# Performance work log

Measured on AMD Instinct MI355X. Metric: run time of the kernel, lower is better.

The kernel has to match this reference:

```python
import jax, jax.numpy as jnp
import numpy as np

B, L, D, V1, V2, V3 = 512, 48, 256, 512, 512, 64


def setup_inputs() -> dict:
    key = jax.random.key(0)
    ks = jax.random.split(key, 20)
    def w(k, shape, fan_in):
        return jax.random.normal(k, shape, dtype=jnp.float32) / np.sqrt(fan_in)
    inp = {
        'x1': jax.random.normal(ks[0], (B, L, V1), dtype=jnp.float32),
        'x2': jax.random.normal(ks[1], (B, L, V2), dtype=jnp.float32),
        's': jax.random.normal(ks[2], (B, V3), dtype=jnp.float32),
        'w_e1': w(ks[3], (D, V1), V1), 'b_e1': jnp.zeros((D,), jnp.float32),
        'w_e2': w(ks[4], (D, V2), V2), 'b_e2': jnp.zeros((D,), jnp.float32),
        'w_s': w(ks[5], (D, V3), V3), 'b_s': jnp.zeros((D,), jnp.float32),
        'w_x': w(ks[6], (1, D), D),                      # mlp_for_x, no bias
        'w_h': w(ks[7], (L, D), D), 'b_h': w(ks[8], (L,), D),  # mlp_for_hidden
        'w_ih': w(ks[9], (3 * D, D), D), 'w_hh': w(ks[10], (3 * D, D), D),
        'b_ih': w(ks[11], (3 * D,), D), 'b_hh': w(ks[12], (3 * D,), D),
        'w_out': w(ks[13], (1, D), D), 'b_out': jnp.zeros((1,), jnp.float32),
    }
    return inp


def _gru_cell(x, h, w_ih, w_hh, b_ih, b_hh):
    # torch GRUCell: gates ordered r, z, n
    gi = x @ w_ih.T + b_ih
    gh = h @ w_hh.T + b_hh
    i_r, i_z, i_n = jnp.split(gi, 3, axis=-1)
    h_r, h_z, h_n = jnp.split(gh, 3, axis=-1)
    r = jax.nn.sigmoid(i_r + h_r)
    z = jax.nn.sigmoid(i_z + h_z)
    n = jnp.tanh(i_n + r * h_n)
    return (1.0 - z) * n + z * h


def reference(x1, x2, s, w_e1, b_e1, w_e2, b_e2, w_s, b_s, w_x, w_h, b_h,
              w_ih, w_hh, b_ih, b_hh, w_out, b_out):
    x1e = jax.nn.relu(jnp.einsum('blv,dv->bld', x1, w_e1) + b_e1)
    x2e = jax.nn.relu(jnp.einsum('blv,dv->bld', x2, w_e2) + b_e2)
    se = s @ w_s.T + b_s                      # [B, D]
    x = x1e + x2e                             # [B, L, D]
    # prefix[:, i] = sum_{j < i} x2e[:, j, 0]  (the torch.where zero test)
    cums = jnp.cumsum(x2e[:, :, 0], axis=1)
    prefix = jnp.concatenate([jnp.zeros((B, 1), x.dtype), cums[:, :-1]], axis=1)  # [B, L]
    idx = jnp.arange(L)

    def step(h, inputs):
        i, pref = inputs                       # i: scalar step, pref: [B]
        le = (idx <= i).astype(x.dtype)        # keep timesteps 0..i (pad rest with 0)
        ip = x * le[None, :, None]             # input_padded [B, L, D]
        lt = (idx < i)
        cond = (pref == 0.0)[:, None]          # batches with zero history in ch0
        guid = jnp.where(idx[None, :] == i, 1.0,
                         jnp.where(cond & lt[None, :], 1.0, 0.0)).astype(x.dtype)  # [B, L]
        gi = ip * guid[:, :, None]
        t1 = jnp.einsum('bld,d->bl', gi, w_x[0]) + (h @ w_h.T + b_h)  # [B, L]
        a = jax.nn.softmax(t1, axis=1)
        ctx = jnp.einsum('bld,bl->bd', ip, a)
        h2 = _gru_cell(ctx, h, w_ih, w_hh, b_ih, b_hh)
        return h2, None

    h0 = jnp.zeros((B, D), x.dtype)
    hF, _ = jax.lax.scan(step, h0, (idx, prefix.T))
    y = jax.nn.sigmoid((hF + se) @ w_out.T + b_out)  # [B, 1]
    return y
```

## Files before the change

### kernel.cpp

```cpp
#include <hip/hip_runtime.h>
#include <stdint.h>

#define B_ 512
#define L_ 48
#define D_ 256

typedef __attribute__((ext_vector_type(8))) short bf16x8;
typedef __attribute__((ext_vector_type(4))) short bf16x4;
typedef __attribute__((ext_vector_type(4))) float f32x4;
typedef __attribute__((ext_vector_type(4))) int i32x4;

__device__ __forceinline__ short f2bf(float f) {
    union { float f; unsigned u; } v; v.f = f;
    unsigned u = v.u;
    unsigned r = (u + 0x7FFFu + ((u >> 16) & 1u)) >> 16;
    return (short)r;
}
__device__ __forceinline__ float bf2f(short s) {
    union { unsigned u; float f; } v; v.u = ((unsigned)(unsigned short)s) << 16;
    return v.f;
}

__global__ __launch_bounds__(256) void k_prep(const float* __restrict__ w_hh,
                                              const float* __restrict__ w_h,
                                              const float* __restrict__ w_ih,
                                              signed char* __restrict__ W1q,
                                              signed char* __restrict__ W2q,
                                              float* __restrict__ qA,
                                              float* __restrict__ qC) {
    int w = threadIdx.x >> 6, lane = threadIdx.x & 63;
    int R = blockIdx.x * 4 + w;
    if (R >= 1584) return;
    const float* src;
    signed char* dst;
    bool isA = (R < 816);
    if (R < 768)      { src = w_hh + (size_t)R * 256;         dst = W1q + (size_t)R * 256; }
    else if (R < 816) { src = w_h + (size_t)(R - 768) * 256;  dst = W1q + (size_t)R * 256; }
    else              { src = w_ih + (size_t)(R - 816) * 256; dst = W2q + (size_t)(R - 816) * 256; }
    float4 v = *(const float4*)(src + lane * 4);
    float m = fmaxf(fmaxf(fabsf(v.x), fabsf(v.y)), fmaxf(fabsf(v.z), fabsf(v.w)));
    #pragma unroll
    for (int o = 32; o; o >>= 1) m = fmaxf(m, __shfl_xor(m, o));
    float sc = (m > 0.f) ? 127.f / m : 0.f;
    int b0 = __float2int_rn(v.x * sc), b1 = __float2int_rn(v.y * sc);
    int b2 = __float2int_rn(v.z * sc), b3 = __float2int_rn(v.w * sc);
    unsigned word = (unsigned)(b0 & 255) | ((unsigned)(b1 & 255) << 8) |
                    ((unsigned)(b2 & 255) << 16) | ((unsigned)(b3 & 255) << 24);
    ((unsigned*)dst)[lane] = word;
    if (lane == 0) {
        if (isA) qA[R] = m / (127.f * 127.f);
        else     qC[R - 816] = m * 8.f / (127.f * 127.f);
    }
}

__device__ __forceinline__ void gemm_pass(const float* __restrict__ X,
                                          const float* __restrict__ W,
                                          short (*sA)[40], short (*sB)[40],
                                          int m0, int n0, int srow, int sseg,
                                          int mf, int nf, int row16, int kg,
                                          f32x4 (&acc)[2][4]) {
    for (int k0 = 0; k0 < 512; k0 += 32) {
        __syncthreads();
        {
            const float* src = X + (size_t)(m0 + srow) * 512 + k0 + sseg * 8;
            float4 p0 = *(const float4*)(src);
            float4 p1 = *(const float4*)(src + 4);
            bf16x8 v;
            v[0] = f2bf(p0.x); v[1] = f2bf(p0.y); v[2] = f2bf(p0.z); v[3] = f2bf(p0.w);
            v[4] = f2bf(p1.x); v[5] = f2bf(p1.y); v[6] = f2bf(p1.z); v[7] = f2bf(p1.w);
            *(bf16x8*)&sA[srow][sseg * 8] = v;
        }
        {
            const float* src = W + (size_t)(n0 + srow) * 512 + k0 + sseg * 8;
            float4 p0 = *(const float4*)(src);
            float4 p1 = *(const float4*)(src + 4);
            bf16x8 v;
            v[0] = f2bf(p0.x); v[1] = f2bf(p0.y); v[2] = f2bf(p0.z); v[3] = f2bf(p0.w);
            v[4] = f2bf(p1.x); v[5] = f2bf(p1.y); v[6] = f2bf(p1.z); v[7] = f2bf(p1.w);
            *(bf16x8*)&sB[srow][sseg * 8] = v;
        }
        __syncthreads();
        bf16x8 a0 = *(bf16x8*)&sA[(mf + 0) * 16 + row16][kg * 8];
        bf16x8 a1 = *(bf16x8*)&sA[(mf + 1) * 16 + row16][kg * 8];
        #pragma unroll
        for (int j = 0; j < 4; ++j) {
            bf16x8 bv = *(bf16x8*)&sB[(nf + j) * 16 + row16][kg * 8];
            acc[0][j] = __builtin_amdgcn_mfma_f32_16x16x32_bf16(a0, bv, acc[0][j], 0, 0, 0);
            acc[1][j] = __builtin_amdgcn_mfma_f32_16x16x32_bf16(a1, bv, acc[1][j], 0, 0, 0);
        }
    }
}

__device__ __forceinline__ void gemm_pass_c0(const float* __restrict__ X,
                                             const float* __restrict__ W,
                                             const float* __restrict__ we2r0,
                                             bool doC0, float& c0acc,
                                             short (*sA)[40], short (*sB)[40],
                                             int m0, int n0, int srow, int sseg,
                                             int mf, int nf, int row16, int kg,
                                             f32x4 (&acc)[2][4]) {
    for (int k0 = 0; k0 < 512; k0 += 32) {
        __syncthreads();
        {
            const float* src = X + (size_t)(m0 + srow) * 512 + k0 + sseg * 8;
            float4 p0 = *(const float4*)(src);
            float4 p1 = *(const float4*)(src + 4);
            if (doC0) {
                const float* wr = we2r0 + k0 + sseg * 8;
                c0acc += p0.x * wr[0] + p0.y * wr[1] + p0.z * wr[2] + p0.w * wr[3]
                       + p1.x * wr[4] + p1.y * wr[5] + p1.z * wr[6] + p1.w * wr[7];
            }
            bf16x8 v;
            v[0] = f2bf(p0.x); v[1] = f2bf(p0.y); v[2] = f2bf(p0.z); v[3] = f2bf(p0.w);
            v[4] = f2bf(p1.x); v[5] = f2bf(p1.y); v[6] = f2bf(p1.z); v[7] = f2bf(p1.w);
            *(bf16x8*)&sA[srow][sseg * 8] = v;
        }
        {
            const float* src = W + (size_t)(n0 + srow) * 512 + k0 + sseg * 8;
            float4 p0 = *(const float4*)(src);
            float4 p1 = *(const float4*)(src + 4);
            bf16x8 v;
            v[0] = f2bf(p0.x); v[1] = f2bf(p0.y); v[2] = f2bf(p0.z); v[3] = f2bf(p0.w);
            v[4] = f2bf(p1.x); v[5] = f2bf(p1.y); v[6] = f2bf(p1.z); v[7] = f2bf(p1.w);
            *(bf16x8*)&sB[srow][sseg * 8] = v;
        }
        __syncthreads();
        bf16x8 a0 = *(bf16x8*)&sA[(mf + 0) * 16 + row16][kg * 8];
        bf16x8 a1 = *(bf16x8*)&sA[(mf + 1) * 16 + row16][kg * 8];
        #pragma unroll
        for (int j = 0; j < 4; ++j) {
            bf16x8 bv = *(bf16x8*)&sB[(nf + j) * 16 + row16][kg * 8];
            acc[0][j] = __builtin_amdgcn_mfma_f32_16x16x32_bf16(a0, bv, acc[0][j], 0, 0, 0);
            acc[1][j] = __builtin_amdgcn_mfma_f32_16x16x32_bf16(a1, bv, acc[1][j], 0, 0, 0);
        }
    }
}

__global__ __launch_bounds__(512) void k_embed(const float* __restrict__ x1,
                                               const float* __restrict__ x2,
                                               const float* __restrict__ w_e1,
                                               const float* __restrict__ b_e1,
                                               const float* __restrict__ w_e2,
                                               const float* __restrict__ b_e2,
                                               short* __restrict__ xb,
                                               float* __restrict__ c0) {
    __shared__ short sA[128][40];
    __shared__ short sB[128][40];
    int bid = blockIdx.x;
    int mt = bid >> 1, nt = bid & 1;
    int m0 = mt * 128, n0 = nt * 128;
    int tid = threadIdx.x;
    int lane = tid & 63, w = tid >> 6;
    int mf = (w & 3) * 2;
    int nf = (w >> 2) * 4;
    int row16 = lane & 15, kg = lane >> 4;
    int srow = tid >> 2, sseg = tid & 3;

    f32x4 acc[2][4], keep[2][4];
    #pragma unroll
    for (int a = 0; a < 2; ++a)
        #pragma unroll
        for (int j = 0; j < 4; ++j) { acc[a][j] = {0.f, 0.f, 0.f, 0.f}; }

    gemm_pass(x1, w_e1, sA, sB, m0, n0, srow, sseg, mf, nf, row16, kg, acc);
    #pragma unroll
    for (int a = 0; a < 2; ++a)
        #pragma unroll
        for (int j = 0; j < 4; ++j) { keep[a][j] = acc[a][j]; acc[a][j] = {0.f, 0.f, 0.f, 0.f}; }

    float c0acc = 0.f;
    const bool doC0 = (nt == 0);
    gemm_pass_c0(x2, w_e2, w_e2, doC0, c0acc, sA, sB, m0, n0, srow, sseg, mf, nf, row16, kg, acc);

    if (doC0) {
        float t = c0acc;
        t += __shfl_xor(t, 1);
        t += __shfl_xor(t, 2);
        if (sseg == 0) c0[m0 + srow] = fmaxf(t + b_e2[0], 0.f);
    }

    #pragma unroll
    for (int a = 0; a < 2; ++a) {
        int mbase = m0 + (mf + a) * 16 + kg * 4;
        #pragma unroll
        for (int j = 0; j < 4; ++j) {
            int n = n0 + (nf + j) * 16 + row16;
            float be1 = b_e1[n], be2 = b_e2[n];
            #pragma unroll
            for (int e = 0; e < 4; ++e) {
                float v1 = fmaxf(keep[a][j][e] + be1, 0.f);
                float v2 = fmaxf(acc[a][j][e] + be2, 0.f);
                xb[(size_t)(mbase + e) * 256 + n] = f2bf(v1 + v2);
            }
        }
    }
}

__global__ __launch_bounds__(256) void k_quant(const short* __restrict__ xb,
                                               const float* __restrict__ w_x,
                                               signed char* __restrict__ xq,
                                               float* __restrict__ xs,
                                               float* __restrict__ xw) {
    int w = threadIdx.x >> 6, lane = threadIdx.x & 63;
    int row = blockIdx.x * 4 + w;
    const short* src = xb + (size_t)row * 256 + lane * 4;
    bf16x4 v = *(const bf16x4*)src;
    float f0 = bf2f(v.x), f1 = bf2f(v.y), f2 = bf2f(v.z), f3 = bf2f(v.w);
    float m = fmaxf(fmaxf(f0, f1), fmaxf(f2, f3));
    float t = f0 * w_x[lane * 4] + f1 * w_x[lane * 4 + 1] +
              f2 * w_x[lane * 4 + 2] + f3 * w_x[lane * 4 + 3];
    #pragma unroll
    for (int o = 32; o; o >>= 1) {
        m = fmaxf(m, __shfl_xor(m, o));
        t += __shfl_xor(t, o);
    }
    float sc = (m > 0.f) ? 127.f / m : 0.f;
    int b0 = __float2int_rn(f0 * sc), b1 = __float2int_rn(f1 * sc);
    int b2 = __float2int_rn(f2 * sc), b3 = __float2int_rn(f3 * sc);
    unsigned word = (unsigned)(b0 & 255) | ((unsigned)(b1 & 255) << 8) |
                    ((unsigned)(b2 & 255) << 16) | ((unsigned)(b3 & 255) << 24);
    ((unsigned*)xq)[(size_t)row * 64 + lane] = word;
    if (lane == 0) { xs[row] = m / 127.f; xw[row] = t; }
}

__global__ __launch_bounds__(256) void k_aux2(const float* __restrict__ c0,
                                              const float* __restrict__ s_in,
                                              const float* __restrict__ w_s,
                                              const float* __restrict__ b_s,
                                              unsigned long long* __restrict__ condbits,
                                              float* __restrict__ se) {
    __shared__ float sS[64];
    int b = blockIdx.x;
    int t = threadIdx.x;
    if (t < 64) sS[t] = s_in[b * 64 + t];
    __syncthreads();
    float acc = b_s[t];
    const float* wr = w_s + t * 64;
    #pragma unroll 8
    for (int kk = 0; kk < 64; ++kk) acc += sS[kk] * wr[kk];
    se[(size_t)b * 256 + t] = acc;
    if (t == 0) {
        unsigned long long bits = 0;
        bool run = true;
        const float* cr = c0 + (size_t)b * 48;
        for (int i = 0; i < 48; ++i) {
            if (run) bits |= (1ull << i);
            run = run && (cr[i] == 0.0f);
        }
        condbits[b] = bits;
    }
}

__device__ __forceinline__ void mfma4r(const i32x4 (&a)[4], const i32x4 (&b)[4], i32x4& acc) {
    #pragma unroll
    for (int s = 0; s < 4; ++s)
        acc = __builtin_amdgcn_mfma_i32_16x16x64_i8(a[s], b[s], acc, 0, 0, 0);
}

__global__ __launch_bounds__(512, 1) void k_scan(const signed char* __restrict__ W1q,
                                                 const signed char* __restrict__ W2q,
                                                 const float* __restrict__ qAg,
                                                 const float* __restrict__ qCg,
                                                 const float* __restrict__ b_hh,
                                                 const float* __restrict__ b_h,
                                                 const float* __restrict__ b_ih,
                                                 const signed char* __restrict__ xq,
                                                 const float* __restrict__ xs,
                                                 const float* __restrict__ xw,
                                                 const unsigned long long* __restrict__ condbits,
                                                 const float* __restrict__ se,
                                                 const float* __restrict__ w_out,
                                                 const float* __restrict__ b_out,
                                                 float* __restrict__ out) {
    __shared__ signed char lWc[8][3][4096];
    __shared__ signed char lWs[3][4096];
    __shared__ signed char lXq[2 * 48 * 256];
    __shared__ signed char lH8[16][272];
    __shared__ signed char lX8[16][272];
    __shared__ float lS[2][52];
    __shared__ float lTw[8][49];
    __shared__ float lbA[816], lqA[816], lbC[768], lqC[768];
    __shared__ float lRed[8][2];

    const int tid = threadIdx.x;
    const int w = tid >> 6, lane = tid & 63;
    const int row16 = lane & 15, kg = lane >> 4;
    const int b0 = blockIdx.x * 2;
    const int g1 = 8 + w;
    const int c0 = w * 16 + row16, c1 = g1 * 16 + row16;
    const int swz = (row16 & 7) << 4;
    const float CS = 127.f / 8.f;
    const int mb = w >> 2;
    const int dimb = ((w & 3) << 6) + lane;

    for (int t = tid; t < 816; t += 512) {
        lbA[t] = (t < 768) ? b_hh[t] : b_h[t - 768];
        lqA[t] = qAg[t];
    }
    for (int t = tid; t < 768; t += 512) { lbC[t] = b_ih[t]; lqC[t] = qCg[t]; }
    for (int t = tid; t < 1088; t += 512) {
        ((int*)lH8)[t] = 0;
        ((int*)lX8)[t] = 0;
    }
    {
        const int4* src = (const int4*)(xq + (size_t)b0 * 48 * 256);
        int4* dst = (int4*)lXq;
        #pragma unroll
        for (int t = 0; t < 3; ++t) dst[tid + t * 512] = src[tid + t * 512];
    }

    const float xwv = (lane < 48) ? xw[(size_t)(b0 + mb) * 48 + lane] : 0.f;
    const float xsv = (lane < 48) ? xs[(size_t)(b0 + mb) * 48 + lane] : 0.f;
    const unsigned long long cbits = condbits[b0 + mb];

    const int fro = row16 * 256 + kg * 16;
    i32x4 wa0[3][4], wa1[3][4], wc0[3][4];
    #pragma unroll
    for (int t = 0; t < 3; ++t) {
        const signed char* p0 = W1q + (size_t)(t * 16 + w) * 4096 + fro;
        const signed char* p1 = W1q + (size_t)(t * 16 + g1) * 4096 + fro;
        const signed char* p2 = W2q + (size_t)(t * 16 + w) * 4096 + fro;
        #pragma unroll
        for (int s = 0; s < 4; ++s) {
            wa0[t][s] = *(const i32x4*)(p0 + s * 64);
            wa1[t][s] = *(const i32x4*)(p1 + s * 64);
            wc0[t][s] = *(const i32x4*)(p2 + s * 64);
        }
    }
    #pragma unroll
    for (int t = 0; t < 3; ++t) {
        const signed char* src = W2q + (size_t)(t * 16 + g1) * 4096 + fro;
        signed char* dst = &lWc[w][t][row16 * 256];
        #pragma unroll
        for (int s = 0; s < 4; ++s)
            *(i32x4*)(dst + ((kg * 16 + s * 64) ^ swz)) = *(const i32x4*)(src + s * 64);
    }
    if (w < 3) {
        const signed char* src = W1q + (size_t)(48 + w) * 4096 + fro;
        signed char* dst = &lWs[w][row16 * 256];
        #pragma unroll
        for (int s = 0; s < 4; ++s)
            *(i32x4*)(dst + ((kg * 16 + s * 64) ^ swz)) = *(const i32x4*)(src + s * 64);
    }
    __syncthreads();

    const signed char* xl = lXq + mb * 12288 + dimb;

    float h0[2] = {0.f, 0.f};
    float h1[2] = {0.f, 0.f};

    for (int i = 0; i < 48; ++i) {
        i32x4 av[4];
        #pragma unroll
        for (int s = 0; s < 4; ++s) av[s] = *(const i32x4*)(&lH8[row16][0] + kg * 16 + s * 64);
        if (w < 3) {
            i32x4 scv = {0,0,0,0};
            #pragma unroll
            for (int s = 0; s < 4; ++s) {
                i32x4 b = *(const i32x4*)(&lWs[w][row16 * 256] + ((kg * 16 + s * 64) ^ swz));
                scv = __builtin_amdgcn_mfma_i32_16x16x64_i8(av[s], b, scv, 0, 0, 0);
            }
            const int n = 768 + w * 16 + row16;
            const float q = lqA[n], bb = lbA[n];
            if (kg == 0) {
                #pragma unroll
                for (int e = 0; e < 2; ++e) lS[e][w * 16 + row16] = (float)scv[e] * q + bb;
            }
        }
        i32x4 aR0 = {0,0,0,0}, aZ0 = {0,0,0,0}, aN0 = {0,0,0,0};
        i32x4 aR1 = {0,0,0,0}, aZ1 = {0,0,0,0}, aN1 = {0,0,0,0};
        mfma4r(av, wa0[0], aR0); mfma4r(av, wa0[1], aZ0); mfma4r(av, wa0[2], aN0);
        mfma4r(av, wa1[0], aR1); mfma4r(av, wa1[1], aZ1); mfma4r(av, wa1[2], aN1);
        __syncthreads();

        {
            float val = -3.0e38f;
            if (lane < 48) {
                val = lS[mb][lane];
                bool cb = (cbits >> i) & 1ull;
                if (lane == i || (cb && lane < i)) val += xwv;
            }
            float mx = val;
            #pragma unroll
            for (int o = 32; o; o >>= 1) mx = fmaxf(mx, __shfl_xor(mx, o));
            float ex = (lane < 48) ? __expf(val - mx) : 0.f;
            float sm = ex;
            #pragma unroll
            for (int o = 32; o; o >>= 1) sm += __shfl_xor(sm, o);
            if (lane < 48) lTw[w][lane] = (ex / sm) * xsv;
        }
        {
            const float* tw = lTw[w];
            float acc = 0.f;
            #pragma unroll 4
            for (int j = 0; j <= i; ++j)
                acc += tw[j] * (float)xl[j * 256];
            lX8[mb][dimb] = (signed char)__float2int_rn(fminf(fmaxf(acc * CS, -127.f), 127.f));
        }
        __syncthreads();

        i32x4 cv[4];
        #pragma unroll
        for (int s = 0; s < 4; ++s) cv[s] = *(const i32x4*)(&lX8[row16][0] + kg * 16 + s * 64);
        {
            i32x4 cr = {0,0,0,0}, cz = {0,0,0,0}, cn = {0,0,0,0};
            mfma4r(cv, wc0[0], cr); mfma4r(cv, wc0[1], cz); mfma4r(cv, wc0[2], cn);
            #pragma unroll
            for (int e = 0; e < 2; ++e) {
                float gr = (float)aR0[e] * lqA[c0]       + lbA[c0]       + (float)cr[e] * lqC[c0]       + lbC[c0];
                float gz = (float)aZ0[e] * lqA[256 + c0] + lbA[256 + c0] + (float)cz[e] * lqC[256 + c0] + lbC[256 + c0];
                float gh = (float)aN0[e] * lqA[512 + c0] + lbA[512 + c0];
                float gn = (float)cn[e] * lqC[512 + c0]  + lbC[512 + c0];
                float r = 1.f / (1.f + __expf(-gr));
                float z = 1.f / (1.f + __expf(-gz));
                float nn = 1.f - 2.f / (__expf(2.f * (gn + r * gh)) + 1.f);
                float hp = (1.f - z) * nn + z * h0[e];
                h0[e] = hp;
                if (kg == 0)
                    lH8[e][c0] = (signed char)__float2int_rn(fminf(fmaxf(hp, -1.f), 1.f) * 127.f);
            }
        }
        {
            i32x4 cr = {0,0,0,0}, cz = {0,0,0,0}, cn = {0,0,0,0};
            #pragma unroll
            for (int s = 0; s < 4; ++s) {
                int off = (kg * 16 + s * 64) ^ swz;
                i32x4 br = *(const i32x4*)(&lWc[w][0][row16 * 256] + off);
                i32x4 bz = *(const i32x4*)(&lWc[w][1][row16 * 256] + off);
                i32x4 bn = *(const i32x4*)(&lWc[w][2][row16 * 256] + off);
                cr = __builtin_amdgcn_mfma_i32_16x16x64_i8(cv[s], br, cr, 0, 0, 0);
                cz = __builtin_amdgcn_mfma_i32_16x16x64_i8(cv[s], bz, cz, 0, 0, 0);
                cn = __builtin_amdgcn_mfma_i32_16x16x64_i8(cv[s], bn, cn, 0, 0, 0);
            }
            #pragma unroll
            for (int e = 0; e < 2; ++e) {
                float gr = (float)aR1[e] * lqA[c1]       + lbA[c1]       + (float)cr[e] * lqC[c1]       + lbC[c1];
                float gz = (float)aZ1[e] * lqA[256 + c1] + lbA[256 + c1] + (float)cz[e] * lqC[256 + c1] + lbC[256 + c1];
                float gh = (float)aN1[e] * lqA[512 + c1] + lbA[512 + c1];
                float gn = (float)cn[e] * lqC[512 + c1]  + lbC[512 + c1];
                float r = 1.f / (1.f + __expf(-gr));
                float z = 1.f / (1.f + __expf(-gz));
                float nn = 1.f - 2.f / (__expf(2.f * (gn + r * gh)) + 1.f);
                float hp = (1.f - z) * nn + z * h1[e];
                h1[e] = hp;
                if (kg == 0)
                    lH8[e][c1] = (signed char)__float2int_rn(fminf(fmaxf(hp, -1.f), 1.f) * 127.f);
            }
        }
        __syncthreads();
    }

    if (kg == 0) {
        float p[2];
        #pragma unroll
        for (int e = 0; e < 2; ++e) {
            int b = b0 + e;
            p[e] = (h0[e] + se[(size_t)b * 256 + c0]) * w_out[c0]
                 + (h1[e] + se[(size_t)b * 256 + c1]) * w_out[c1];
        }
        #pragma unroll
        for (int o = 1; o < 16; o <<= 1) {
            #pragma unroll
            for (int e = 0; e < 2; ++e) p[e] += __shfl_xor(p[e], o);
        }
        if (row16 == 0) {
            #pragma unroll
            for (int e = 0; e < 2; ++e) lRed[w][e] = p[e];
        }
    }
    __syncthreads();
    if (tid < 2) {
        float sum = 0.f;
        #pragma unroll
        for (int q = 0; q < 8; ++q) sum += lRed[q][tid];
        out[b0 + tid] = 1.f / (1.f + __expf(-(sum + b_out[0])));
    }
}

extern "C" void kernel_launch(void* const* d_in, const int* in_sizes, int n_in,
                              void* d_out, int out_size, void* d_ws, size_t ws_size,
                              hipStream_t stream) {
    const float* x1   = (const float*)d_in[0];
    const float* x2   = (const float*)d_in[1];
    const float* s    = (const float*)d_in[2];
    const float* w_e1 = (const float*)d_in[3];
    const float* b_e1 = (const float*)d_in[4];
    const float* w_e2 = (const float*)d_in[5];
    const float* b_e2 = (const float*)d_in[6];
    const float* w_s  = (const float*)d_in[7];
    const float* b_s  = (const float*)d_in[8];
    const float* w_x  = (const float*)d_in[9];
    const float* w_h  = (const float*)d_in[10];
    const float* b_h  = (const float*)d_in[11];
    const float* w_ih = (const float*)d_in[12];
    const float* w_hh = (const float*)d_in[13];
    const float* b_ih = (const float*)d_in[14];
    const float* b_hh = (const float*)d_in[15];
    const float* w_out = (const float*)d_in[16];
    const float* b_out = (const float*)d_in[17];
    float* out = (float*)d_out;

    char* ws = (char*)d_ws;
    size_t off = 0;
    auto alloc = [&](size_t bytes) -> void* {
        void* p = ws + off;
        off = (off + bytes + 255) & ~(size_t)255;
        return p;
    };
    short* xb = (short*)alloc((size_t)B_ * L_ * D_ * 2);
    signed char* xq = (signed char*)alloc((size_t)B_ * L_ * D_);
    float* xs = (float*)alloc((size_t)B_ * L_ * 4);
    signed char* W1q = (signed char*)alloc(896 * 256);
    signed char* W2q = (signed char*)alloc(768 * 256);
    float* qA = (float*)alloc(816 * 4);
    float* qC = (float*)alloc(768 * 4);
    float* c0 = (float*)alloc((size_t)B_ * L_ * 4);
    float* xw = (float*)alloc((size_t)B_ * L_ * 4);
    unsigned long long* cb = (unsigned long long*)alloc(B_ * 8);
    float* se = (float*)alloc((size_t)B_ * D_ * 4);

    hipLaunchKernelGGL(k_prep, dim3(396), dim3(256), 0, stream,
                       w_hh, w_h, w_ih, W1q, W2q, qA, qC);
    hipLaunchKernelGGL(k_embed, dim3(384), dim3(512), 0, stream,
                       x1, x2, w_e1, b_e1, w_e2, b_e2, xb, c0);
    hipLaunchKernelGGL(k_quant, dim3(6144), dim3(256), 0, stream,
                       xb, w_x, xq, xs, xw);
    hipLaunchKernelGGL(k_aux2, dim3(512), dim3(256), 0, stream,
                       c0, s, w_s, b_s, cb, se);
    hipLaunchKernelGGL(k_scan, dim3(256), dim3(512), 0, stream,
                       W1q, W2q, qA, qC, b_hh, b_h, b_ih, xq, xs, xw, cb, se,
                       w_out, b_out, out);
}
```

Measured before the change: 235.7 us.

## Compute attention scores redundantly per wave and transpose x cache to drop a barrier

Every wave now computes the three score MFMAs itself and pulls the values out with lane shuffles, instead of waves 0-2 writing scores to shared memory. This removes one __syncthreads per timestep. The int8 input cache is stored transposed, [batch][dim][time], so the context sum can read four timesteps as one packed int and pair them with a float4 of weights. In exchange each wave issues redundant MFMAs and shared-memory weight loads, and the strided global transpose in the prologue is slower.

```diff
diff --git a/kernel.cpp b/kernel.cpp
--- a/kernel.cpp
+++ b/kernel.cpp
@@ -274,11 +274,10 @@
                                                  float* __restrict__ out) {
     __shared__ signed char lWc[8][3][4096];
     __shared__ signed char lWs[3][4096];
-    __shared__ signed char lXq[2 * 48 * 256];
+    __shared__ signed char lXqT[2][256][52];
     __shared__ signed char lH8[16][272];
     __shared__ signed char lX8[16][272];
-    __shared__ float lS[2][52];
-    __shared__ float lTw[8][49];
+    __shared__ float lTw[8][52];
     __shared__ float lbA[816], lqA[816], lbC[768], lqC[768];
     __shared__ float lRed[8][2];
 
@@ -303,14 +302,17 @@
         ((int*)lX8)[t] = 0;
     }
     {
-        const int4* src = (const int4*)(xq + (size_t)b0 * 48 * 256);
-        int4* dst = (int4*)lXq;
-        #pragma unroll
-        for (int t = 0; t < 3; ++t) dst[tid + t * 512] = src[tid + t * 512];
+        int bq = tid >> 8, dq = tid & 255;
+        const signed char* src = xq + (size_t)(b0 + bq) * 12288 + dq;
+        signed char* dst = &lXqT[bq][dq][0];
+        #pragma unroll
+        for (int j = 0; j < 48; ++j) dst[j] = src[(size_t)j * 256];
     }
 
     const float xwv = (lane < 48) ? xw[(size_t)(b0 + mb) * 48 + lane] : 0.f;
     const float xsv = (lane < 48) ? xs[(size_t)(b0 + mb) * 48 + lane] : 0.f;
+    const float qsv = (lane < 48) ? qAg[768 + lane] : 0.f;
+    const float bsv = (lane < 48) ? b_h[lane] : 0.f;
     const unsigned long long cbits = condbits[b0 + mb];
 
     const int fro = row16 * 256 + kg * 16;
@@ -344,8 +346,6 @@
     }
     __syncthreads();
 
-    const signed char* xl = lXq + mb * 12288 + dimb;
-
     float h0[2] = {0.f, 0.f};
     float h1[2] = {0.f, 0.f};
 
@@ -353,30 +353,36 @@
         i32x4 av[4];
         #pragma unroll
         for (int s = 0; s < 4; ++s) av[s] = *(const i32x4*)(&lH8[row16][0] + kg * 16 + s * 64);
-        if (w < 3) {
-            i32x4 scv = {0,0,0,0};
-            #pragma unroll
-            for (int s = 0; s < 4; ++s) {
-                i32x4 b = *(const i32x4*)(&lWs[w][row16 * 256] + ((kg * 16 + s * 64) ^ swz));
-                scv = __builtin_amdgcn_mfma_i32_16x16x64_i8(av[s], b, scv, 0, 0, 0);
-            }
-            const int n = 768 + w * 16 + row16;
-            const float q = lqA[n], bb = lbA[n];
-            if (kg == 0) {
-                #pragma unroll
-                for (int e = 0; e < 2; ++e) lS[e][w * 16 + row16] = (float)scv[e] * q + bb;
-            }
+        i32x4 sv0 = {0,0,0,0}, sv1 = {0,0,0,0}, sv2 = {0,0,0,0};
+        #pragma unroll
+        for (int s = 0; s < 4; ++s) {
+            int off = (kg * 16 + s * 64) ^ swz;
+            i32x4 q0 = *(const i32x4*)(&lWs[0][row16 * 256] + off);
+            i32x4 q1 = *(const i32x4*)(&lWs[1][row16 * 256] + off);
+            i32x4 q2 = *(const i32x4*)(&lWs[2][row16 * 256] + off);
+            sv0 = __builtin_amdgcn_mfma_i32_16x16x64_i8(av[s], q0, sv0, 0, 0, 0);
+            sv1 = __builtin_amdgcn_mfma_i32_16x16x64_i8(av[s], q1, sv1, 0, 0, 0);
+            sv2 = __builtin_amdgcn_mfma_i32_16x16x64_i8(av[s], q2, sv2, 0, 0, 0);
         }
         i32x4 aR0 = {0,0,0,0}, aZ0 = {0,0,0,0}, aN0 = {0,0,0,0};
         i32x4 aR1 = {0,0,0,0}, aZ1 = {0,0,0,0}, aN1 = {0,0,0,0};
         mfma4r(av, wa0[0], aR0); mfma4r(av, wa0[1], aZ0); mfma4r(av, wa0[2], aN0);
         mfma4r(av, wa1[0], aR1); mfma4r(av, wa1[1], aZ1); mfma4r(av, wa1[2], aN1);
-        __syncthreads();
-
-        {
+
+        {
+            float e00 = (float)sv0[0], e10 = (float)sv0[1];
+            float e01 = (float)sv1[0], e11 = (float)sv1[1];
+            float e02 = (float)sv2[0], e12 = (float)sv2[1];
+            float s0 = mb ? e10 : e00;
+            float s1 = mb ? e11 : e01;
+            float s2 = mb ? e12 : e02;
+            float v0 = __shfl(s0, row16);
+            float v1 = __shfl(s1, row16);
+            float v2 = __shfl(s2, row16);
+            float raw = (lane < 16) ? v0 : ((lane < 32) ? v1 : v2);
             float val = -3.0e38f;
             if (lane < 48) {
-                val = lS[mb][lane];
+                val = raw * qsv + bsv;
                 bool cb = (cbits >> i) & 1ull;
                 if (lane == i || (cb && lane < i)) val += xwv;
             }
@@ -391,10 +397,17 @@
         }
         {
             const float* tw = lTw[w];
+            const signed char* xv = &lXqT[mb][dimb][0];
             float acc = 0.f;
-            #pragma unroll 4
-            for (int j = 0; j <= i; ++j)
-                acc += tw[j] * (float)xl[j * 256];
+            int j = 0;
+            for (; j + 3 <= i; j += 4) {
+                union { int v; signed char c[4]; } pk;
+                pk.v = *(const int*)(xv + j);
+                float4 t4 = *(const float4*)(tw + j);
+                acc += t4.x * (float)pk.c[0] + t4.y * (float)pk.c[1]
+                     + t4.z * (float)pk.c[2] + t4.w * (float)pk.c[3];
+            }
+            for (; j <= i; ++j) acc += tw[j] * (float)xv[j];
             lX8[mb][dimb] = (signed char)__float2int_rn(fminf(fmaxf(acc * CS, -127.f), 127.f));
         }
         __syncthreads();
```

After: 231.2 us, median of 2. About the same (-1.9%).
